# Kernel tuning notes

Measured on AMD Instinct MI355X. Metric: run time of the kernel, lower is better.

The kernel has to match this reference:

```python
import jax, jax.numpy as jnp
import numpy as np
import math

INPUT_SZ = 512
HIDDEN_SZ = 1024


def setup_inputs() -> dict:
    key = jax.random.key(0)
    ks = jax.random.split(key, 13)
    stdv = 1.0 / math.sqrt(HIDDEN_SZ)

    def u(k, shape):
        return jax.random.uniform(k, shape, jnp.float32, -stdv, stdv)

    x = jax.random.normal(ks[0], (32, 512, INPUT_SZ), jnp.float32)
    names = ['f', 'i', 'o', 'g']
    inp = {'x': x}
    ki = 1
    for n in names:
        inp[f'U_{n}'] = u(ks[ki], (INPUT_SZ, HIDDEN_SZ)); ki += 1
        inp[f'V_{n}'] = u(ks[ki], (HIDDEN_SZ, HIDDEN_SZ)); ki += 1
        inp[f'b_{n}'] = u(ks[ki], (HIDDEN_SZ,)); ki += 1
    return inp


def reference(x, U_f, V_f, b_f, U_i, V_i, b_i, U_o, V_o, b_o, U_g, V_g, b_g):
    bs, seq_sz, _ = x.shape
    hid = V_f.shape[0]
    # Precompute all input projections for the 4 gates in one pass (parallel over time).
    U = jnp.concatenate([U_f, U_i, U_o, U_g], axis=1)        # [in, 4H]
    V = jnp.concatenate([V_f, V_i, V_o, V_g], axis=1)        # [H, 4H]
    b = jnp.concatenate([b_f, b_i, b_o, b_g], axis=0)        # [4H]
    xU = jnp.einsum('bti,ih->bth', x, U) + b                 # [bs, T, 4H]

    def step(carry, xu_t):
        h_t, c_t = carry
        gates = xu_t + h_t @ V                               # [bs, 4H]
        f_t = jax.nn.sigmoid(gates[:, 0 * hid:1 * hid])
        i_t = jax.nn.sigmoid(gates[:, 1 * hid:2 * hid])
        o_t = jax.nn.sigmoid(gates[:, 2 * hid:3 * hid])
        g_t = jnp.tanh(gates[:, 3 * hid:4 * hid])
        c_t = f_t * c_t + i_t * g_t
        h_t = o_t * jnp.tanh(c_t)
        return (h_t, c_t), h_t

    h0 = jnp.zeros((bs, hid), x.dtype)
    c0 = jnp.zeros((bs, hid), x.dtype)
    (h_last, _), hs = jax.lax.scan(step, (h0, c0), jnp.swapaxes(xU, 0, 1))
    hidden_seq = jnp.swapaxes(hs, 0, 1)                      # [bs, T, H]
    return h_last, hidden_seq
```

## Files before the change

### kernel.cpp

```cpp
#include <hip/hip_runtime.h>


typedef __bf16 bf16x8 __attribute__((ext_vector_type(8)));
typedef float f32x16 __attribute__((ext_vector_type(16)));

#define NWG 64
#define T_STEPS 512
#define HID 1024
#define BS 32
#define WS_FULL 126877696

__device__ __forceinline__ unsigned short f2bf(float f) {
  unsigned int u = __float_as_uint(f);
  u = (u + 0x7FFFu + ((u >> 16) & 1u)) >> 16;
  return (unsigned short)u;
}
__device__ __forceinline__ float b2f(unsigned short s) {
  return __uint_as_float(((unsigned int)s) << 16);
}
__device__ __forceinline__ float sigm(float v) {
  v = fminf(fmaxf(v, -30.f), 30.f);
  return 1.f / (1.f + __expf(-v));
}
__device__ __forceinline__ float tanh_(float v) {
  v = fminf(fmaxf(v, -15.f), 15.f);
  float e = __expf(-2.f * v);
  return (1.f - e) / (1.f + e);
}

__global__ void cvt_x_kernel(const float* __restrict__ x,
                             unsigned int* __restrict__ xfH,
                             unsigned int* __restrict__ xfL) {
  const int t = blockIdx.x;
  const int tid = threadIdx.x;
  __shared__ float xs[32 * 512];
  {
    const int b = tid >> 3;
    const int k0 = (tid & 7) * 64;
    const float* src = x + ((size_t)(b * 512 + t)) * 512 + k0;
    for (int i = 0; i < 64; i += 4) {
      float4 v = *reinterpret_cast<const float4*>(src + i);
      xs[b * 512 + k0 + i + 0] = v.x;
      xs[b * 512 + k0 + i + 1] = v.y;
      xs[b * 512 + k0 + i + 2] = v.z;
      xs[b * 512 + k0 + i + 3] = v.w;
    }
  }
  __syncthreads();
  unsigned int* dH = xfH + (size_t)t * 8192;
  unsigned int* dL = xfL + (size_t)t * 8192;
  for (int i = 0; i < 32; ++i) {
    int idx = i * 256 + tid;
    int kt = idx >> 8;
    int pos = idx & 255;
    int lane = pos >> 2;
    int r = pos & 3;
    int kk = 8 * (lane >> 5) + 2 * r;
    int b2 = lane & 31;
    float f0 = xs[b2 * 512 + kt * 16 + kk];
    float f1 = xs[b2 * 512 + kt * 16 + kk + 1];
    unsigned short h0 = f2bf(f0), h1 = f2bf(f1);
    unsigned short l0 = f2bf(f0 - b2f(h0)), l1 = f2bf(f1 - b2f(h1));
    dH[idx] = (unsigned int)h0 | ((unsigned int)h1 << 16);
    dL[idx] = (unsigned int)l0 | ((unsigned int)l1 << 16);
  }
}

__global__ void cvt_uv_kernel(const float* Uf, const float* Vf,
                              const float* Ui, const float* Vi,
                              const float* Uo, const float* Vo,
                              const float* Ug, const float* Vg,
                              unsigned int* __restrict__ vfH,
                              unsigned int* __restrict__ vfL,
                              unsigned int* __restrict__ ufH,
                              unsigned int* __restrict__ ufL) {
  int blk = blockIdx.x;
  int kt = blk % 96;
  int nt = (blk / 96) & 1;
  int wg = blk / 192;
  int lane = threadIdx.x;
  int col32 = lane & 31;
  int c64 = nt * 32 + col32;
  int gate = c64 >> 4;
  int jg = wg * 16 + (c64 & 15);
  const float* V_ = (gate == 0) ? Vf : (gate == 1) ? Vi : (gate == 2) ? Vo : Vg;
  const float* U_ = (gate == 0) ? Uf : (gate == 1) ? Ui : (gate == 2) ? Uo : Ug;
  for (int r = 0; r < 4; ++r) {
    int kk = 8 * (lane >> 5) + 2 * r;
    if (kt < 64) {
      int K = kt * 16 + kk;
      float f0 = V_[(size_t)K * HID + jg];
      float f1 = V_[(size_t)(K + 1) * HID + jg];
      unsigned short h0 = f2bf(f0), h1 = f2bf(f1);
      unsigned short l0 = f2bf(f0 - b2f(h0)), l1 = f2bf(f1 - b2f(h1));
      size_t idx = ((size_t)(wg * 2 + nt) * 64 + kt) * 256 + lane * 4 + r;
      vfH[idx] = (unsigned int)h0 | ((unsigned int)h1 << 16);
      vfL[idx] = (unsigned int)l0 | ((unsigned int)l1 << 16);
    } else {
      int K = (kt - 64) * 16 + kk;
      float f0 = U_[(size_t)K * HID + jg];
      float f1 = U_[(size_t)(K + 1) * HID + jg];
      unsigned short h0 = f2bf(f0), h1 = f2bf(f1);
      unsigned short l0 = f2bf(f0 - b2f(h0)), l1 = f2bf(f1 - b2f(h1));
      size_t idx = ((size_t)(wg * 2 + nt) * 32 + (kt - 64)) * 256 + lane * 4 + r;
      ufH[idx] = (unsigned int)h0 | ((unsigned int)h1 << 16);
      ufL[idx] = (unsigned int)l0 | ((unsigned int)l1 << 16);
    }
  }
}

__device__ __forceinline__ int gidx(int nt, int w, int row, int col) {
  return ((nt * 8 + w) * 32 + row) * 32 + (col ^ row);
}

__global__ __launch_bounds__(512, 2) void lstm_main(
    const unsigned short* __restrict__ ufragH,
    const unsigned short* __restrict__ ufragL,
    const unsigned short* __restrict__ vfragH,
    const unsigned short* __restrict__ vfragL,
    const unsigned short* __restrict__ xfragH,
    const unsigned short* __restrict__ xfragL,
    unsigned int* hfH, unsigned int* hfL, unsigned int* flags,
    const float* __restrict__ bfv, const float* __restrict__ biv,
    const float* __restrict__ bov, const float* __restrict__ bgv) {
  __shared__ unsigned short ldsU[2 * 32 * 512];
  __shared__ float gbuf[2 * 8 * 32 * 32];

  const int wg = blockIdx.x;
  const int tid = threadIdx.x;
  const int lane = tid & 63;
  const int w = tid >> 6;

  {
    const bf16x8* src = reinterpret_cast<const bf16x8*>(ufragH + (size_t)wg * 32768);
    bf16x8* dst = reinterpret_cast<bf16x8*>(ldsU);
    for (int i = 0; i < 8; ++i) dst[i * 512 + tid] = src[i * 512 + tid];
  }
  __syncthreads();
  __builtin_amdgcn_fence(__ATOMIC_ACQUIRE, "agent");

  bf16x8 uL[2][4], vH[2][8], vL[2][8];
#pragma unroll
  for (int nt = 0; nt < 2; ++nt) {
    const bf16x8* bl = reinterpret_cast<const bf16x8*>(ufragL + (size_t)wg * 32768) +
                       (size_t)nt * 32 * 64;
#pragma unroll
    for (int p = 0; p < 4; ++p) uL[nt][p] = bl[(w * 4 + p) * 64 + lane];
    const bf16x8* vh =
        reinterpret_cast<const bf16x8*>(vfragH + (size_t)((wg * 2 + nt) * 64) * 512);
    const bf16x8* vl =
        reinterpret_cast<const bf16x8*>(vfragL + (size_t)((wg * 2 + nt) * 64) * 512);
#pragma unroll
    for (int q = 0; q < 8; ++q) {
      vH[nt][q] = vh[(w * 8 + q) * 64 + lane];
      vL[nt][q] = vl[(w * 8 + q) * 64 + lane];
    }
  }

  const int b_ = tid & 31;
  const int jp_ = (tid >> 5) & 7;
  const int jg0 = wg * 16 + 2 * jp_;
  const float Bf0 = bfv[jg0], Bf1 = bfv[jg0 + 1];
  const float Bi0 = biv[jg0], Bi1 = biv[jg0 + 1];
  const float Bo0 = bov[jg0], Bo1 = bov[jg0 + 1];
  const float Bg0 = bgv[jg0], Bg1 = bgv[jg0 + 1];
  float c0 = 0.f, c1 = 0.f;
  const int hw = wg * 256 + (b_ + 32 * (jp_ >> 2)) * 4 + (jp_ & 3);

#pragma unroll 1
  for (int t = 0; t < T_STEPS; ++t) {
    f32x16 acc0 = {};
    f32x16 acc1 = {};

    {
      const bf16x8* axh = reinterpret_cast<const bf16x8*>(xfragH + (size_t)t * 16384);
      const bf16x8* axl = reinterpret_cast<const bf16x8*>(xfragL + (size_t)t * 16384);
      const bf16x8* lu = reinterpret_cast<const bf16x8*>(ldsU);
#pragma unroll
      for (int p = 0; p < 4; ++p) {
        int ktx = w * 4 + p;
        bf16x8 ah = axh[ktx * 64 + lane];
        bf16x8 al = axl[ktx * 64 + lane];
        bf16x8 u0 = lu[ktx * 64 + lane];
        bf16x8 u1 = lu[(32 + ktx) * 64 + lane];
        acc0 = __builtin_amdgcn_mfma_f32_32x32x16_bf16(ah, u0, acc0, 0, 0, 0);
        acc0 = __builtin_amdgcn_mfma_f32_32x32x16_bf16(ah, uL[0][p], acc0, 0, 0, 0);
        acc0 = __builtin_amdgcn_mfma_f32_32x32x16_bf16(al, u0, acc0, 0, 0, 0);
        acc1 = __builtin_amdgcn_mfma_f32_32x32x16_bf16(ah, u1, acc1, 0, 0, 0);
        acc1 = __builtin_amdgcn_mfma_f32_32x32x16_bf16(ah, uL[1][p], acc1, 0, 0, 0);
        acc1 = __builtin_amdgcn_mfma_f32_32x32x16_bf16(al, u1, acc1, 0, 0, 0);
      }
    }

    if (t > 0) {
      if (lane < 8) {
        while (__hip_atomic_load(&flags[w * 8 + lane], __ATOMIC_RELAXED,
                                 __HIP_MEMORY_SCOPE_AGENT) < (unsigned int)t) {
        }
      }
      const bf16x8* ahh = reinterpret_cast<const bf16x8*>(
          reinterpret_cast<const unsigned short*>(hfH) + (size_t)(t - 1) * 32768);
      const bf16x8* ahl = reinterpret_cast<const bf16x8*>(
          reinterpret_cast<const unsigned short*>(hfL) + (size_t)(t - 1) * 32768);
      bf16x8 aH[8], aL[8];
#pragma unroll
      for (int q = 0; q < 8; ++q) {
        aH[q] = ahh[(w * 8 + q) * 64 + lane];
        aL[q] = ahl[(w * 8 + q) * 64 + lane];
      }
#pragma unroll
      for (int q = 0; q < 8; ++q) {
        acc0 = __builtin_amdgcn_mfma_f32_32x32x16_bf16(aH[q], vH[0][q], acc0, 0, 0, 0);
        acc0 = __builtin_amdgcn_mfma_f32_32x32x16_bf16(aH[q], vL[0][q], acc0, 0, 0, 0);
        acc0 = __builtin_amdgcn_mfma_f32_32x32x16_bf16(aL[q], vH[0][q], acc0, 0, 0, 0);
        acc1 = __builtin_amdgcn_mfma_f32_32x32x16_bf16(aH[q], vH[1][q], acc1, 0, 0, 0);
        acc1 = __builtin_amdgcn_mfma_f32_32x32x16_bf16(aH[q], vL[1][q], acc1, 0, 0, 0);
        acc1 = __builtin_amdgcn_mfma_f32_32x32x16_bf16(aL[q], vH[1][q], acc1, 0, 0, 0);
      }
    }

    {
      const int colw = lane & 31;
      const int rbase = 4 * (lane >> 5);
#pragma unroll
      for (int r = 0; r < 16; ++r) {
        int row = (r & 3) + 8 * (r >> 2) + rbase;
        gbuf[gidx(0, w, row, colw)] = acc0[r];
        gbuf[gidx(1, w, row, colw)] = acc1[r];
      }
    }
    __syncthreads();

    if (tid < 256) {
      const int jl0 = 2 * jp_, jl1 = jl0 + 1;
      float gf0 = Bf0, gf1 = Bf1, gi0 = Bi0, gi1 = Bi1;
      float go0 = Bo0, go1 = Bo1, gg0 = Bg0, gg1 = Bg1;
#pragma unroll
      for (int ww = 0; ww < 8; ++ww) {
        gf0 += gbuf[gidx(0, ww, b_, jl0)];
        gf1 += gbuf[gidx(0, ww, b_, jl1)];
        gi0 += gbuf[gidx(0, ww, b_, 16 + jl0)];
        gi1 += gbuf[gidx(0, ww, b_, 16 + jl1)];
        go0 += gbuf[gidx(1, ww, b_, jl0)];
        go1 += gbuf[gidx(1, ww, b_, jl1)];
        gg0 += gbuf[gidx(1, ww, b_, 16 + jl0)];
        gg1 += gbuf[gidx(1, ww, b_, 16 + jl1)];
      }
      c0 = sigm(gf0) * c0 + sigm(gi0) * tanh_(gg0);
      c1 = sigm(gf1) * c1 + sigm(gi1) * tanh_(gg1);
      float h0 = sigm(go0) * tanh_(c0);
      float h1 = sigm(go1) * tanh_(c1);
      unsigned short h0h = f2bf(h0), h1h = f2bf(h1);
      unsigned short h1l = f2bf(h1 - b2f(h1h));
      unsigned short h0l = f2bf(h0 - b2f(h0h));
      unsigned int hvH = (unsigned int)h0h | ((unsigned int)h1h << 16);
      unsigned int hvL = (unsigned int)h0l | ((unsigned int)h1l << 16);
      size_t base = (size_t)t * 16384 + hw;
      __hip_atomic_store(&hfH[base], hvH, __ATOMIC_RELAXED,
                         __HIP_MEMORY_SCOPE_AGENT);
      __hip_atomic_store(&hfL[base], hvL, __ATOMIC_RELAXED,
                         __HIP_MEMORY_SCOPE_AGENT);
    }
    __syncthreads();
    if (tid == 0) {
      __hip_atomic_store(&flags[wg], (unsigned int)(t + 1), __ATOMIC_RELAXED,
                         __HIP_MEMORY_SCOPE_AGENT);
    }
  }
}

__global__ __launch_bounds__(256) void expand_out(
    const unsigned int* __restrict__ hfH, const unsigned int* __restrict__ hfL,
    float* __restrict__ out) {
  __builtin_amdgcn_fence(__ATOMIC_ACQUIRE, "agent");
  const int tid = threadIdx.x;
#pragma unroll
  for (int i = 0; i < 4; ++i) {
    size_t g = (size_t)blockIdx.x * 1024 + i * 256 + tid;
    int t = (int)(g >> 14);
    int d = (int)(g & 16383);
    int wg = d >> 8;
    int off = d & 255;
    int lane_h = off >> 2;
    int r_h = off & 3;
    int b = lane_h & 31;
    int jp = (lane_h >> 5) * 4 + r_h;
    int j0 = wg * 16 + 2 * jp;
    unsigned int uH = hfH[g];
    unsigned int uL = hfL[g];
    float f0 = b2f((unsigned short)(uH & 0xFFFF)) + b2f((unsigned short)(uL & 0xFFFF));
    float f1 = b2f((unsigned short)(uH >> 16)) + b2f((unsigned short)(uL >> 16));
    float2 v = make_float2(f0, f1);
    *reinterpret_cast<float2*>(out + 32768 + ((size_t)(b * T_STEPS + t)) * HID + j0) = v;
    if (t == T_STEPS - 1) {
      *reinterpret_cast<float2*>(out + (size_t)b * HID + j0) = v;
    }
  }
}

__global__ __launch_bounds__(256) void r9_step_gemm(
    const float* __restrict__ x, const float* __restrict__ hbuf,
    const float* __restrict__ Vf, const float* __restrict__ Vi,
    const float* __restrict__ Vo, const float* __restrict__ Vg,
    const float* __restrict__ Uf, const float* __restrict__ Ui,
    const float* __restrict__ Uo, const float* __restrict__ Ug,
    float* __restrict__ P, int t) {
  const int kb = blockIdx.x;
  const int cb = blockIdx.y;
  const int tidx = threadIdx.x;
  const int gate = cb >> 2;
  const int j = (cb & 3) * 256 + tidx;
  const int col = cb * 256 + tidx;
  const float* V_ = (gate == 0) ? Vf : (gate == 1) ? Vi : (gate == 2) ? Vo : Vg;
  const float* U_ = (gate == 0) ? Uf : (gate == 1) ? Ui : (gate == 2) ? Uo : Ug;
  __shared__ float hs[BS][32];
  __shared__ float xs2[BS][32];
  {
    int idx = tidx * 4;
#pragma unroll
    for (int i = 0; i < 4; ++i, ++idx) {
      int b = idx >> 5, u = idx & 31;
      hs[b][u] = hbuf[b * HID + kb * 32 + u];
      if (kb < 16) xs2[b][u] = x[((size_t)b * T_STEPS + t) * 512 + kb * 32 + u];
    }
  }
  __syncthreads();
  float acc[BS];
#pragma unroll
  for (int b = 0; b < BS; ++b) acc[b] = 0.f;
  const float* vp = V_ + (size_t)(kb * 32) * HID + j;
#pragma unroll 4
  for (int k = 0; k < 32; ++k) {
    float vv = vp[(size_t)k * HID];
#pragma unroll
    for (int b = 0; b < BS; ++b) acc[b] += hs[b][k] * vv;
  }
  if (kb < 16) {
    const float* up = U_ + (size_t)(kb * 32) * HID + j;
#pragma unroll 4
    for (int k = 0; k < 32; ++k) {
      float uv = up[(size_t)k * HID];
#pragma unroll
      for (int b = 0; b < BS; ++b) acc[b] += xs2[b][k] * uv;
    }
  }
  float* pp = P + (size_t)kb * BS * 4096 + col;
#pragma unroll
  for (int b = 0; b < BS; ++b) pp[(size_t)b * 4096] = acc[b];
}

__global__ __launch_bounds__(256) void r9_step_cell(
    const float* __restrict__ P,
    const float* __restrict__ bfv, const float* __restrict__ biv,
    const float* __restrict__ bov, const float* __restrict__ bgv,
    float* __restrict__ hbuf, float* __restrict__ cbuf,
    float* __restrict__ out, int t) {
  const int idx = blockIdx.x * 256 + threadIdx.x;
  const int b = idx >> 10, j = idx & 1023;
  float gf = bfv[j], gi = biv[j], go = bov[j], gg = bgv[j];
  const float* pb = P + (size_t)b * 4096;
#pragma unroll 8
  for (int kb = 0; kb < 32; ++kb) {
    const float* pk = pb + (size_t)kb * BS * 4096;
    gf += pk[j];
    gi += pk[1024 + j];
    go += pk[2048 + j];
    gg += pk[3072 + j];
  }
  float fs = sigm(gf), is = sigm(gi), os = sigm(go), gt = tanh_(gg);
  float c = fs * cbuf[idx] + is * gt;
  cbuf[idx] = c;
  float h = os * tanh_(c);
  hbuf[idx] = h;
  out[32768 + ((size_t)b * T_STEPS + t) * HID + j] = h;
  if (t == T_STEPS - 1) out[(size_t)b * HID + j] = h;
}

extern "C" void kernel_launch(void* const* d_in, const int* in_sizes, int n_in,
                              void* d_out, int out_size, void* d_ws, size_t ws_size,
                              hipStream_t stream) {
  const float *x, *Uf, *Vf, *bf, *Ui, *Vi, *bi, *Uo, *Vo, *bo, *Ug, *Vg, *bg;
  float* out = (float*)d_out;

  bool okA = (n_in == 13) && in_sizes[0] == 8388608 && in_sizes[1] == 524288 &&
             in_sizes[2] == 1048576 && in_sizes[3] == 1024 &&
             in_sizes[4] == 524288 && in_sizes[7] == 524288 &&
             in_sizes[10] == 524288 && in_sizes[12] == 1024;
  if (okA) {
    x = (const float*)d_in[0];
    Uf = (const float*)d_in[1];  Vf = (const float*)d_in[2];  bf = (const float*)d_in[3];
    Ui = (const float*)d_in[4];  Vi = (const float*)d_in[5];  bi = (const float*)d_in[6];
    Uo = (const float*)d_in[7];  Vo = (const float*)d_in[8];  bo = (const float*)d_in[9];
    Ug = (const float*)d_in[10]; Vg = (const float*)d_in[11]; bg = (const float*)d_in[12];
  } else {
    Uf = (const float*)d_in[0];  Ug = (const float*)d_in[1];
    Ui = (const float*)d_in[2];  Uo = (const float*)d_in[3];
    Vf = (const float*)d_in[4];  Vg = (const float*)d_in[5];
    Vi = (const float*)d_in[6];  Vo = (const float*)d_in[7];
    bf = (const float*)d_in[8];  bg = (const float*)d_in[9];
    bi = (const float*)d_in[10]; bo = (const float*)d_in[11];
    x = (const float*)d_in[12];
  }

  char* ws = (char*)d_ws;
  if (ws_size >= (size_t)WS_FULL) {
    unsigned int* flags = (unsigned int*)(ws + 0);
    unsigned int* vfragH = (unsigned int*)(ws + 1048576);
    unsigned int* vfragL = (unsigned int*)(ws + 9437184);
    unsigned int* ufragH = (unsigned int*)(ws + 17825792);
    unsigned int* ufragL = (unsigned int*)(ws + 22020096);
    unsigned int* xfragH = (unsigned int*)(ws + 26214400);
    unsigned int* xfragL = (unsigned int*)(ws + 42991616);
    unsigned int* hfH = (unsigned int*)(ws + 59768832);
    unsigned int* hfL = (unsigned int*)(ws + 93323264);

    (void)hipMemsetAsync(flags, 0, 4096, stream);
    cvt_uv_kernel<<<64 * 2 * 96, 64, 0, stream>>>(Uf, Vf, Ui, Vi, Uo, Vo, Ug, Vg,
                                                  vfragH, vfragL, ufragH, ufragL);
    cvt_x_kernel<<<512, 256, 0, stream>>>(x, xfragH, xfragL);
    lstm_main<<<NWG, 512, 0, stream>>>(
        (unsigned short*)ufragH, (unsigned short*)ufragL, (unsigned short*)vfragH,
        (unsigned short*)vfragL, (unsigned short*)xfragH, (unsigned short*)xfragL,
        hfH, hfL, flags, bf, bi, bo, bg);
    expand_out<<<8192, 256, 0, stream>>>(hfH, hfL, out);
  } else {
    float* P = (float*)ws;
    float* hbuf = (float*)(ws + 16777216);
    float* cbuf = (float*)(ws + 16908288);
    (void)hipMemsetAsync(hbuf, 0, 131072, stream);
    (void)hipMemsetAsync(cbuf, 0, 131072, stream);
    for (int t = 0; t < T_STEPS; ++t) {
      r9_step_gemm<<<dim3(32, 16), 256, 0, stream>>>(x, hbuf, Vf, Vi, Vo, Vg, Uf, Ui,
                                                     Uo, Ug, P, t);
      r9_step_cell<<<128, 256, 0, stream>>>(P, bf, bi, bo, bg, hbuf, cbuf, out, t);
    }
  }
}
```

Measured before the change: 3.916 ms.

## Use per-wave completion flags, double-buffer gate LDS, keep U fragments in registers

Each of the four writer waves now publishes its own progress flag after waiting for its h stores, so the trailing block barrier and single-thread flag store are gone. Consumers poll 32 per-wave flags instead of 8 per-block flags. The gate reduction buffer is double-buffered by step parity so the next step's writes cannot race the previous step's reads without a second barrier. U high fragments move from LDS into registers, with launch bounds relaxed to one block per CU to allow the extra register pressure.

```diff
diff --git a/kernel.cpp b/kernel.cpp
--- a/kernel.cpp
+++ b/kernel.cpp
@@ -113,39 +113,35 @@
   return ((nt * 8 + w) * 32 + row) * 32 + (col ^ row);
 }
 
-__global__ __launch_bounds__(512, 2) void lstm_main(
+__global__ __launch_bounds__(512, 1) void lstm_main(
     const unsigned short* __restrict__ ufragH,
     const unsigned short* __restrict__ ufragL,
     const unsigned short* __restrict__ vfragH,
     const unsigned short* __restrict__ vfragL,
     const unsigned short* __restrict__ xfragH,
     const unsigned short* __restrict__ xfragL,
-    unsigned int* hfH, unsigned int* hfL, unsigned int* flags,
+    unsigned int* hfH, unsigned int* hfL, unsigned int* flags4,
     const float* __restrict__ bfv, const float* __restrict__ biv,
     const float* __restrict__ bov, const float* __restrict__ bgv) {
-  __shared__ unsigned short ldsU[2 * 32 * 512];
-  __shared__ float gbuf[2 * 8 * 32 * 32];
+  __shared__ float gbuf[2 * 16384];
 
   const int wg = blockIdx.x;
   const int tid = threadIdx.x;
   const int lane = tid & 63;
   const int w = tid >> 6;
 
-  {
-    const bf16x8* src = reinterpret_cast<const bf16x8*>(ufragH + (size_t)wg * 32768);
-    bf16x8* dst = reinterpret_cast<bf16x8*>(ldsU);
-    for (int i = 0; i < 8; ++i) dst[i * 512 + tid] = src[i * 512 + tid];
-  }
-  __syncthreads();
   __builtin_amdgcn_fence(__ATOMIC_ACQUIRE, "agent");
 
-  bf16x8 uL[2][4], vH[2][8], vL[2][8];
+  bf16x8 uH[2][4], uL[2][4], vH[2][8], vL[2][8];
 #pragma unroll
   for (int nt = 0; nt < 2; ++nt) {
-    const bf16x8* bl = reinterpret_cast<const bf16x8*>(ufragL + (size_t)wg * 32768) +
-                       (size_t)nt * 32 * 64;
-#pragma unroll
-    for (int p = 0; p < 4; ++p) uL[nt][p] = bl[(w * 4 + p) * 64 + lane];
+    const bf16x8* bh = reinterpret_cast<const bf16x8*>(ufragH + (size_t)wg * 32768);
+    const bf16x8* bl = reinterpret_cast<const bf16x8*>(ufragL + (size_t)wg * 32768);
+#pragma unroll
+    for (int p = 0; p < 4; ++p) {
+      uH[nt][p] = bh[(nt * 32 + w * 4 + p) * 64 + lane];
+      uL[nt][p] = bl[(nt * 32 + w * 4 + p) * 64 + lane];
+    }
     const bf16x8* vh =
         reinterpret_cast<const bf16x8*>(vfragH + (size_t)((wg * 2 + nt) * 64) * 512);
     const bf16x8* vl =
@@ -175,26 +171,24 @@
     {
       const bf16x8* axh = reinterpret_cast<const bf16x8*>(xfragH + (size_t)t * 16384);
       const bf16x8* axl = reinterpret_cast<const bf16x8*>(xfragL + (size_t)t * 16384);
-      const bf16x8* lu = reinterpret_cast<const bf16x8*>(ldsU);
 #pragma unroll
       for (int p = 0; p < 4; ++p) {
         int ktx = w * 4 + p;
         bf16x8 ah = axh[ktx * 64 + lane];
         bf16x8 al = axl[ktx * 64 + lane];
-        bf16x8 u0 = lu[ktx * 64 + lane];
-        bf16x8 u1 = lu[(32 + ktx) * 64 + lane];
-        acc0 = __builtin_amdgcn_mfma_f32_32x32x16_bf16(ah, u0, acc0, 0, 0, 0);
+        acc0 = __builtin_amdgcn_mfma_f32_32x32x16_bf16(ah, uH[0][p], acc0, 0, 0, 0);
         acc0 = __builtin_amdgcn_mfma_f32_32x32x16_bf16(ah, uL[0][p], acc0, 0, 0, 0);
-        acc0 = __builtin_amdgcn_mfma_f32_32x32x16_bf16(al, u0, acc0, 0, 0, 0);
-        acc1 = __builtin_amdgcn_mfma_f32_32x32x16_bf16(ah, u1, acc1, 0, 0, 0);
+        acc0 = __builtin_amdgcn_mfma_f32_32x32x16_bf16(al, uH[0][p], acc0, 0, 0, 0);
+        acc1 = __builtin_amdgcn_mfma_f32_32x32x16_bf16(ah, uH[1][p], acc1, 0, 0, 0);
         acc1 = __builtin_amdgcn_mfma_f32_32x32x16_bf16(ah, uL[1][p], acc1, 0, 0, 0);
-        acc1 = __builtin_amdgcn_mfma_f32_32x32x16_bf16(al, u1, acc1, 0, 0, 0);
+        acc1 = __builtin_amdgcn_mfma_f32_32x32x16_bf16(al, uH[1][p], acc1, 0, 0, 0);
       }
     }
 
     if (t > 0) {
-      if (lane < 8) {
-        while (__hip_atomic_load(&flags[w * 8 + lane], __ATOMIC_RELAXED,
+      if (lane < 32) {
+        const int pidx = (w * 8 + (lane >> 2)) * 4 + (lane & 3);
+        while (__hip_atomic_load(&flags4[pidx], __ATOMIC_RELAXED,
                                  __HIP_MEMORY_SCOPE_AGENT) < (unsigned int)t) {
         }
       }
@@ -220,39 +214,40 @@
     }
 
     {
+      const int par = (t & 1) * 16384;
       const int colw = lane & 31;
       const int rbase = 4 * (lane >> 5);
 #pragma unroll
       for (int r = 0; r < 16; ++r) {
         int row = (r & 3) + 8 * (r >> 2) + rbase;
-        gbuf[gidx(0, w, row, colw)] = acc0[r];
-        gbuf[gidx(1, w, row, colw)] = acc1[r];
+        gbuf[par + gidx(0, w, row, colw)] = acc0[r];
+        gbuf[par + gidx(1, w, row, colw)] = acc1[r];
       }
     }
     __syncthreads();
 
     if (tid < 256) {
+      const int par = (t & 1) * 16384;
       const int jl0 = 2 * jp_, jl1 = jl0 + 1;
       float gf0 = Bf0, gf1 = Bf1, gi0 = Bi0, gi1 = Bi1;
       float go0 = Bo0, go1 = Bo1, gg0 = Bg0, gg1 = Bg1;
 #pragma unroll
       for (int ww = 0; ww < 8; ++ww) {
-        gf0 += gbuf[gidx(0, ww, b_, jl0)];
-        gf1 += gbuf[gidx(0, ww, b_, jl1)];
-        gi0 += gbuf[gidx(0, ww, b_, 16 + jl0)];
-        gi1 += gbuf[gidx(0, ww, b_, 16 + jl1)];
-        go0 += gbuf[gidx(1, ww, b_, jl0)];
-        go1 += gbuf[gidx(1, ww, b_, jl1)];
-        gg0 += gbuf[gidx(1, ww, b_, 16 + jl0)];
-        gg1 += gbuf[gidx(1, ww, b_, 16 + jl1)];
+        gf0 += gbuf[par + gidx(0, ww, b_, jl0)];
+        gf1 += gbuf[par + gidx(0, ww, b_, jl1)];
+        gi0 += gbuf[par + gidx(0, ww, b_, 16 + jl0)];
+        gi1 += gbuf[par + gidx(0, ww, b_, 16 + jl1)];
+        go0 += gbuf[par + gidx(1, ww, b_, jl0)];
+        go1 += gbuf[par + gidx(1, ww, b_, jl1)];
+        gg0 += gbuf[par + gidx(1, ww, b_, 16 + jl0)];
+        gg1 += gbuf[par + gidx(1, ww, b_, 16 + jl1)];
       }
       c0 = sigm(gf0) * c0 + sigm(gi0) * tanh_(gg0);
       c1 = sigm(gf1) * c1 + sigm(gi1) * tanh_(gg1);
       float h0 = sigm(go0) * tanh_(c0);
       float h1 = sigm(go1) * tanh_(c1);
       unsigned short h0h = f2bf(h0), h1h = f2bf(h1);
-      unsigned short h1l = f2bf(h1 - b2f(h1h));
-      unsigned short h0l = f2bf(h0 - b2f(h0h));
+      unsigned short h0l = f2bf(h0 - b2f(h0h)), h1l = f2bf(h1 - b2f(h1h));
       unsigned int hvH = (unsigned int)h0h | ((unsigned int)h1h << 16);
       unsigned int hvL = (unsigned int)h0l | ((unsigned int)h1l << 16);
       size_t base = (size_t)t * 16384 + hw;
@@ -260,11 +255,11 @@
                          __HIP_MEMORY_SCOPE_AGENT);
       __hip_atomic_store(&hfL[base], hvL, __ATOMIC_RELAXED,
                          __HIP_MEMORY_SCOPE_AGENT);
-    }
-    __syncthreads();
-    if (tid == 0) {
-      __hip_atomic_store(&flags[wg], (unsigned int)(t + 1), __ATOMIC_RELAXED,
-                         __HIP_MEMORY_SCOPE_AGENT);
+      asm volatile("s_waitcnt vmcnt(0)" ::: "memory");
+      if ((tid & 63) == 0) {
+        __hip_atomic_store(&flags4[wg * 4 + (tid >> 6)], (unsigned int)(t + 1),
+                           __ATOMIC_RELAXED, __HIP_MEMORY_SCOPE_AGENT);
+      }
     }
   }
 }
@@ -404,7 +399,7 @@
 
   char* ws = (char*)d_ws;
   if (ws_size >= (size_t)WS_FULL) {
-    unsigned int* flags = (unsigned int*)(ws + 0);
+    unsigned int* flags4 = (unsigned int*)(ws + 0);
     unsigned int* vfragH = (unsigned int*)(ws + 1048576);
     unsigned int* vfragL = (unsigned int*)(ws + 9437184);
     unsigned int* ufragH = (unsigned int*)(ws + 17825792);
@@ -414,14 +409,14 @@
     unsigned int* hfH = (unsigned int*)(ws + 59768832);
     unsigned int* hfL = (unsigned int*)(ws + 93323264);
 
-    (void)hipMemsetAsync(flags, 0, 4096, stream);
+    (void)hipMemsetAsync(flags4, 0, 4096, stream);
     cvt_uv_kernel<<<64 * 2 * 96, 64, 0, stream>>>(Uf, Vf, Ui, Vi, Uo, Vo, Ug, Vg,
                                                   vfragH, vfragL, ufragH, ufragL);
     cvt_x_kernel<<<512, 256, 0, stream>>>(x, xfragH, xfragL);
     lstm_main<<<NWG, 512, 0, stream>>>(
         (unsigned short*)ufragH, (unsigned short*)ufragL, (unsigned short*)vfragH,
         (unsigned short*)vfragL, (unsigned short*)xfragH, (unsigned short*)xfragL,
-        hfH, hfL, flags, bf, bi, bo, bg);
+        hfH, hfL, flags4, bf, bi, bo, bg);
     expand_out<<<8192, 256, 0, stream>>>(hfH, hfL, out);
   } else {
     float* P = (float*)ws;
```

After: 5.899 ms. 1.51x slower.
